# Kernel tuning notes

Hardware: AMD Instinct MI355X
Metric: run time of the kernel (lower is better)

The kernel has to match this reference:

```python
import jax, jax.numpy as jnp
import numpy as np

BETA = 0.35

def setup_inputs() -> dict:
    key = jax.random.key(0)
    k1, k2, k3 = jax.random.split(key, 3)
    B, D, C, O = 16384, 512, 4096, 128
    x = jax.random.normal(k1, (B, D), dtype=jnp.float32)
    centers = jax.random.normal(k2, (C, D), dtype=jnp.float32)
    W = jax.random.normal(k3, (C, O), dtype=jnp.float32) * (1.0 / np.sqrt(C))
    b = jnp.zeros((O,), dtype=jnp.float32)
    return {"x": x, "centers": centers, "W": W, "b": b}

def reference(x, centers, W, b):
    # Squared Euclidean distances via the GEMM identity ||a-b||^2 = ||a||^2 + ||b||^2 - 2 a.b
    # (same math as expand_dims/subtract/square/reduce_sum, avoids [B,C,D] intermediate)
    x_sq = jnp.sum(x * x, axis=1, keepdims=True)          # [B,1]
    c_sq = jnp.sum(centers * centers, axis=1)             # [C]
    cross = x @ centers.T                                  # [B,C]
    sq_dist = x_sq + c_sq[None, :] - 2.0 * cross           # [B,C]
    rbf = jnp.exp(-BETA * sq_dist)                         # [B,C]
    return rbf @ W + b                                      # [B,O]
```

## Files before the change

### kernel.cpp

```cpp
#include <hip/hip_runtime.h>
#include <hip/hip_bf16.h>

typedef short bf16x8 __attribute__((ext_vector_type(8)));
typedef float f32x4 __attribute__((ext_vector_type(4)));
typedef float f32x16 __attribute__((ext_vector_type(16)));
typedef long l64x2 __attribute__((ext_vector_type(2)));
typedef unsigned short u16;
typedef unsigned char u8;

#define NB2 (-0.35f * 1.44269504088896340736f)
#define P2C (0.70f * 1.44269504088896340736f)
#define MF8(a,b,c)  __builtin_amdgcn_mfma_f32_32x32x16_fp8_fp8(a, b, c, 0, 0, 0)
#define MFB(a,b,c)  __builtin_amdgcn_mfma_f32_32x32x16_bf16(a, b, c, 0, 0, 0)

__device__ __forceinline__ u16 f2bf(float f) {
  union { float f; unsigned int u; } v; v.f = f;
  unsigned int x = v.u;
  return (u16)((x + 0x7FFFu + ((x >> 16) & 1u)) >> 16);
}

__device__ __forceinline__ unsigned cvtpk(float lo, float hi) {
  unsigned r;
  asm("v_cvt_pk_bf16_f32 %0, %1, %2" : "=v"(r) : "v"(lo), "v"(hi));
  return r;
}

__device__ __forceinline__ void pswap(unsigned &a, unsigned &b) {
  asm volatile("v_permlane32_swap_b32 %0, %1" : "+v"(a), "+v"(b));
}

__device__ __forceinline__ u8 f2e4m3(float f) {
  unsigned int u = __float_as_uint(f);
  u8 s = (u8)((u >> 24) & 0x80u);
  float a = fabsf(f);
  if (a >= 448.f) return s | 0x7E;
  if (a < 0.015625f) return s | (u8)(int)rintf(a * 512.f);
  unsigned int m = u & 0x7fffffffu;
  unsigned int r = m + 0x7FFFFu + ((m >> 20) & 1u);
  return s | (u8)((((r >> 23) - 120u) << 3) | ((r >> 20) & 7u));
}

__device__ __forceinline__ unsigned int pk4(float a, float b, float c, float d) {
#if __has_builtin(__builtin_amdgcn_cvt_pk_fp8_f32)
  int v = __builtin_amdgcn_cvt_pk_fp8_f32(a, b, 0, false);
  v = __builtin_amdgcn_cvt_pk_fp8_f32(c, d, v, true);
  return (unsigned int)v;
#else
  return (unsigned int)f2e4m3(a) | ((unsigned int)f2e4m3(b) << 8)
       | ((unsigned int)f2e4m3(c) << 16) | ((unsigned int)f2e4m3(d) << 24);
#endif
}

#define GLOAD_LDS(g, l) __builtin_amdgcn_global_load_lds( \
    (const __attribute__((address_space(1))) unsigned int*)(g), \
    (__attribute__((address_space(3))) unsigned int*)(l), 16, 0, 0)

__global__ __launch_bounds__(512)
void prep_x8(const float* __restrict__ src, u8* __restrict__ dst,
             float* __restrict__ sq) {
  const int row = blockIdx.x * 8 + (threadIdx.x >> 6);
  const int i6 = threadIdx.x & 63;
  const float4* p = (const float4*)(src + (size_t)row * 512) + i6 * 2;
  float4 a = p[0], b = p[1];
  float ss = a.x*a.x + a.y*a.y + a.z*a.z + a.w*a.w
           + b.x*b.x + b.y*b.y + b.z*b.z + b.w*b.w;
  uint2 o;
  o.x = pk4(a.x, a.y, a.z, a.w);
  o.y = pk4(b.x, b.y, b.z, b.w);
  const int pp = i6 >> 2, sub = (i6 >> 1) & 1, h = i6 & 1;
  const int l = (h << 5) | (row & 31);
  *(uint2*)(dst + (size_t)(row >> 5) * 16384 + pp * 1024 + l * 16 + sub * 8) = o;
  ss += __shfl_xor(ss, 1);  ss += __shfl_xor(ss, 2);
  ss += __shfl_xor(ss, 4);  ss += __shfl_xor(ss, 8);
  ss += __shfl_xor(ss, 16); ss += __shfl_xor(ss, 32);
  if (i6 == 0) sq[row] = ss;
}

__global__ __launch_bounds__(256)
void prep_cen(const float* __restrict__ cen, u8* __restrict__ cfr,
              float* __restrict__ csq) {
  const int t = threadIdx.x;
  const int c = blockIdx.x * 4 + (t >> 6);
  const int i6 = t & 63;
  const float* p = cen + (size_t)c * 512 + i6 * 8;
  float4 a = *(const float4*)p, b = *(const float4*)(p + 4);
  float ss = a.x*a.x + a.y*a.y + a.z*a.z + a.w*a.w
           + b.x*b.x + b.y*b.y + b.z*b.z + b.w*b.w;
  uint2 o;
  o.x = pk4(a.x, a.y, a.z, a.w);
  o.y = pk4(b.x, b.y, b.z, b.w);
  const int pp = i6 >> 2, sub = (i6 >> 1) & 1, h = i6 & 1;
  const int lc = c & 31;
  const int v = (((lc & 7) * 2 + h) ^ ((lc >> 2) & 1));
  *(uint2*)(cfr + (size_t)(c >> 5) * 16384 + pp * 1024 + (lc >> 3) * 256
            + v * 16 + sub * 8) = o;
  ss += __shfl_xor(ss, 1);  ss += __shfl_xor(ss, 2);
  ss += __shfl_xor(ss, 4);  ss += __shfl_xor(ss, 8);
  ss += __shfl_xor(ss, 16); ss += __shfl_xor(ss, 32);
  if (i6 == 0) csq[c] = ss;
}

__global__ __launch_bounds__(256)
void prep_w(const float* __restrict__ W, u8* __restrict__ wt) {
  __shared__ u16 t_[128 * 66];
  const int c0 = blockIdx.x * 64;
  const int t = threadIdx.x;
#pragma unroll
  for (int it = 0; it < 32; ++it) {
    int idx = it * 256 + t;
    int cl = idx >> 7;
    int o  = idx & 127;
    t_[o * 66 + cl] = f2bf(W[(size_t)(c0 + cl) * 128 + o]);
  }
  __syncthreads();
#pragma unroll
  for (int it = 0; it < 4; ++it) {
    int idx = it * 256 + t;
    int o  = idx >> 3;
    int uu = idx & 7;
    int ch = uu >> 2;
    int kt = (uu >> 1) & 1;
    int h2 = uu & 1;
    int u  = (kt * 2 + h2) ^ ((o >> 1) & 3);
    u16* d = (u16*)(wt + ((size_t)(c0 >> 5) + ch) * 8192 + o * 64 + u * 16);
    const u16* s_ = &t_[o * 66 + ch * 32 + kt * 16 + h2 * 8];
#pragma unroll
    for (int j = 0; j < 8; ++j) d[j] = s_[j];
  }
}

__global__ __launch_bounds__(256)
void init_out(const float* __restrict__ bias, float* __restrict__ out) {
  const int i4 = blockIdx.x * 256 + threadIdx.x;
  float4 b = ((const float4*)bias)[i4 & 31];
  ((float4*)out)[i4] = b;
}

__global__ __launch_bounds__(256, 2)
void rbf_main(const u8* __restrict__ xfs, const u8* __restrict__ cfr,
              const u8* __restrict__ wtgb, const float* __restrict__ csq_g,
              const float* __restrict__ xsq_g, float* __restrict__ out)
{
  __shared__ __align__(16) u8 cs[2][16384];
  __shared__ __align__(16) u8 wt[2][8192];
  __shared__ __align__(16) float csq_l[1024];
  __shared__ __align__(16) float xsq_l[128];

  const int tid = threadIdx.x;
  const int lane = tid & 63;
  const int wv = tid >> 6;
  const int l31 = lane & 31;
  const int h = lane >> 5;
  const int bid = blockIdx.x;
  const int chq = bid & 3;
  const size_t r0 = (size_t)(bid >> 2) * 128;

#define S_CS(cc) do { \
    const u8* sG_ = cfr + ((size_t)(chq * 32 + (cc)) << 14) + tid * 16; \
    u8* sL_ = &cs[(cc) & 1][0] + tid * 16; \
    GLOAD_LDS(sG_,         sL_); \
    GLOAD_LDS(sG_ + 4096,  sL_ + 4096); \
    GLOAD_LDS(sG_ + 8192,  sL_ + 8192); \
    GLOAD_LDS(sG_ + 12288, sL_ + 12288); \
  } while (0)

#define S_W(cc) do { \
    const u8* wg_ = wtgb + ((size_t)(chq * 32 + (cc)) << 13) + tid * 16; \
    u8* wl_ = &wt[(cc) & 1][0] + tid * 16; \
    GLOAD_LDS(wg_,        wl_); \
    GLOAD_LDS(wg_ + 4096, wl_ + 4096); \
  } while (0)

  if (tid < 32) GLOAD_LDS(xsq_g + r0 + tid * 4, xsq_l + tid * 4);
  GLOAD_LDS(csq_g + chq * 1024 + tid * 4, csq_l + tid * 4);
  S_CS(0);
  S_W(0);

  l64x2 xf[16];
  {
    const u8* xb = xfs + ((size_t)((bid >> 2) * 4 + wv)) * 16384 + lane * 16;
#pragma unroll
    for (int p = 0; p < 16; ++p)
      xf[p] = *(const l64x2*)(xb + p * 1024);
  }

  asm volatile("s_waitcnt vmcnt(0)" ::: "memory");
  __builtin_amdgcn_s_barrier();
  __builtin_amdgcn_sched_barrier(0);

  const float xn = NB2 * xsq_l[wv * 32 + l31];

  const int cbase = ((l31 >> 3) & 3) * 256
                  + ((((l31 & 7) * 2 + h) ^ ((l31 >> 2) & 1)) << 4);
  const int wsw = (l31 >> 1) & 3;
  const int wb_o = l31 * 64;
  const int wu0 = ((0 + h) ^ wsw) << 4;
  const int wu1 = ((2 + h) ^ wsw) << 4;

  const f32x16 z16 = {0,0,0,0,0,0,0,0,0,0,0,0,0,0,0,0};
  f32x16 oa0 = z16, oa1 = z16, oa2 = z16, oa3 = z16;

#pragma unroll 1
  for (int cc = 0; cc < 32; ++cc) {
    if (cc < 31) { S_CS(cc + 1); S_W(cc + 1); }
    const u8* csb = &cs[cc & 1][0];

    f32x16 s0 = z16, s1 = z16;
#pragma unroll
    for (int p = 0; p < 16; ++p) {
      l64x2 A = *(const l64x2*)(csb + p * 1024 + cbase);
      __builtin_amdgcn_s_setprio(1);
      if (p & 1) {
        s1 = MF8(A[0], xf[p][0], s1);
        s1 = MF8(A[1], xf[p][1], s1);
      } else {
        s0 = MF8(A[0], xf[p][0], s0);
        s0 = MF8(A[1], xf[p][1], s0);
      }
      __builtin_amdgcn_s_setprio(0);
    }

    f32x4 cq0 = *(const f32x4*)(csq_l + cc * 32 + 0  + 4 * h);
    f32x4 cq1 = *(const f32x4*)(csq_l + cc * 32 + 8  + 4 * h);
    f32x4 cq2 = *(const f32x4*)(csq_l + cc * 32 + 16 + 4 * h);
    f32x4 cq3 = *(const f32x4*)(csq_l + cc * 32 + 24 + 4 * h);
    float e[16];
#pragma unroll
    for (int r = 0; r < 16; ++r) {
      const float cq = (r < 4 ? cq0[r] : r < 8 ? cq1[r - 4] : r < 12 ? cq2[r - 8] : cq3[r - 12]);
      e[r] = __builtin_amdgcn_exp2f(fmaf(s0[r] + s1[r], P2C, fmaf(cq, NB2, xn)));
    }
    unsigned P0 = cvtpk(e[0],  e[1]),  P1 = cvtpk(e[2],  e[3]);
    unsigned P2 = cvtpk(e[4],  e[5]),  P3 = cvtpk(e[6],  e[7]);
    unsigned P4 = cvtpk(e[8],  e[9]),  P5 = cvtpk(e[10], e[11]);
    unsigned P6 = cvtpk(e[12], e[13]), P7 = cvtpk(e[14], e[15]);
    pswap(P0, P2); pswap(P1, P3);
    pswap(P4, P6); pswap(P5, P7);
    union { unsigned u[4]; bf16x8 v; } FA, GA;
    FA.u[0] = P0; FA.u[1] = P1; FA.u[2] = P2; FA.u[3] = P3;
    GA.u[0] = P4; GA.u[1] = P5; GA.u[2] = P6; GA.u[3] = P7;

    {
      const u8* wtb = &wt[cc & 1][0];
      bf16x8 wA0 = *(const bf16x8*)(wtb + wb_o + wu0);
      bf16x8 wB0 = *(const bf16x8*)(wtb + wb_o + wu1);
      bf16x8 wA1 = *(const bf16x8*)(wtb + 2048 + wb_o + wu0);
      bf16x8 wB1 = *(const bf16x8*)(wtb + 2048 + wb_o + wu1);
      __builtin_amdgcn_s_setprio(1);
      oa0 = MFB(FA.v, wA0, oa0);
      oa0 = MFB(GA.v, wB0, oa0);
      oa1 = MFB(FA.v, wA1, oa1);
      oa1 = MFB(GA.v, wB1, oa1);
      __builtin_amdgcn_s_setprio(0);
      bf16x8 wA2 = *(const bf16x8*)(wtb + 4096 + wb_o + wu0);
      bf16x8 wB2 = *(const bf16x8*)(wtb + 4096 + wb_o + wu1);
      bf16x8 wA3 = *(const bf16x8*)(wtb + 6144 + wb_o + wu0);
      bf16x8 wB3 = *(const bf16x8*)(wtb + 6144 + wb_o + wu1);
      __builtin_amdgcn_s_setprio(1);
      oa2 = MFB(FA.v, wA2, oa2);
      oa2 = MFB(GA.v, wB2, oa2);
      oa3 = MFB(FA.v, wA3, oa3);
      oa3 = MFB(GA.v, wB3, oa3);
      __builtin_amdgcn_s_setprio(0);
    }

    asm volatile("s_waitcnt vmcnt(0)" ::: "memory");
    __builtin_amdgcn_s_barrier();
    __builtin_amdgcn_sched_barrier(0);
  }

#pragma unroll
  for (int r = 0; r < 16; ++r) {
    const int m = wv * 32 + (r & 3) + 8 * (r >> 2) + 4 * h;
    float* op = &out[(r0 + m) * 128 + l31];
    atomicAdd(op,      oa0[r]);
    atomicAdd(op + 32, oa1[r]);
    atomicAdd(op + 64, oa2[r]);
    atomicAdd(op + 96, oa3[r]);
  }
#undef S_CS
#undef S_W
}

extern "C" void kernel_launch(void* const* d_in, const int* in_sizes, int n_in,
                              void* d_out, int out_size, void* d_ws, size_t ws_size,
                              hipStream_t stream) {
  (void)in_sizes; (void)n_in; (void)out_size; (void)ws_size;
  const float* x   = (const float*)d_in[0];
  const float* cen = (const float*)d_in[1];
  const float* W   = (const float*)d_in[2];
  const float* b   = (const float*)d_in[3];
  u8* xfs = (u8*)d_ws;
  u8* cfr = xfs + (size_t)16384 * 512;
  u8* wtgb = cfr + (size_t)4096 * 512;
  float* csq = (float*)(wtgb + (size_t)128 * 4096 * 2);
  float* xsq = csq + 4096;
  prep_x8<<<2048, 512, 0, stream>>>(x, xfs, xsq);
  prep_cen<<<1024, 256, 0, stream>>>(cen, cfr, csq);
  prep_w<<<64, 256, 0, stream>>>(W, wtgb);
  init_out<<<2048, 256, 0, stream>>>(b, (float*)d_out);
  rbf_main<<<512, 256, 0, stream>>>(xfs, cfr, wtgb, csq, xsq, (float*)d_out);
}
```

Before: 105.9 us.

## Load W fragments directly into registers and triple-buffer center tiles in LDS

```diff
diff --git a/kernel.cpp b/kernel.cpp
--- a/kernel.cpp
+++ b/kernel.cpp
@@ -120,10 +120,10 @@
     int uu = idx & 7;
     int ch = uu >> 2;
     int kt = (uu >> 1) & 1;
-    int h2 = uu & 1;
-    int u  = (kt * 2 + h2) ^ ((o >> 1) & 3);
-    u16* d = (u16*)(wt + ((size_t)(c0 >> 5) + ch) * 8192 + o * 64 + u * 16);
-    const u16* s_ = &t_[o * 66 + ch * 32 + kt * 16 + h2 * 8];
+    int h  = uu & 1;
+    u16* d = (u16*)(wt + ((size_t)(c0 >> 5) + ch) * 8192 + (o >> 5) * 2048
+                    + kt * 1024 + (h * 32 + (o & 31)) * 16);
+    const u16* s_ = &t_[o * 66 + ch * 32 + kt * 16 + h * 8];
 #pragma unroll
     for (int j = 0; j < 8; ++j) d[j] = s_[j];
   }
@@ -141,8 +141,7 @@
               const u8* __restrict__ wtgb, const float* __restrict__ csq_g,
               const float* __restrict__ xsq_g, float* __restrict__ out)
 {
-  __shared__ __align__(16) u8 cs[2][16384];
-  __shared__ __align__(16) u8 wt[2][8192];
+  __shared__ __align__(16) u8 cs[3][16384];
   __shared__ __align__(16) float csq_l[1024];
   __shared__ __align__(16) float xsq_l[128];
 
@@ -157,24 +156,17 @@
 
 #define S_CS(cc) do { \
     const u8* sG_ = cfr + ((size_t)(chq * 32 + (cc)) << 14) + tid * 16; \
-    u8* sL_ = &cs[(cc) & 1][0] + tid * 16; \
+    u8* sL_ = &cs[(cc) % 3][0] + tid * 16; \
     GLOAD_LDS(sG_,         sL_); \
     GLOAD_LDS(sG_ + 4096,  sL_ + 4096); \
     GLOAD_LDS(sG_ + 8192,  sL_ + 8192); \
     GLOAD_LDS(sG_ + 12288, sL_ + 12288); \
   } while (0)
 
-#define S_W(cc) do { \
-    const u8* wg_ = wtgb + ((size_t)(chq * 32 + (cc)) << 13) + tid * 16; \
-    u8* wl_ = &wt[(cc) & 1][0] + tid * 16; \
-    GLOAD_LDS(wg_,        wl_); \
-    GLOAD_LDS(wg_ + 4096, wl_ + 4096); \
-  } while (0)
-
   if (tid < 32) GLOAD_LDS(xsq_g + r0 + tid * 4, xsq_l + tid * 4);
   GLOAD_LDS(csq_g + chq * 1024 + tid * 4, csq_l + tid * 4);
   S_CS(0);
-  S_W(0);
+  S_CS(1);
 
   l64x2 xf[16];
   {
@@ -192,18 +184,26 @@
 
   const int cbase = ((l31 >> 3) & 3) * 256
                   + ((((l31 & 7) * 2 + h) ^ ((l31 >> 2) & 1)) << 4);
-  const int wsw = (l31 >> 1) & 3;
-  const int wb_o = l31 * 64;
-  const int wu0 = ((0 + h) ^ wsw) << 4;
-  const int wu1 = ((2 + h) ^ wsw) << 4;
 
   const f32x16 z16 = {0,0,0,0,0,0,0,0,0,0,0,0,0,0,0,0};
   f32x16 oa0 = z16, oa1 = z16, oa2 = z16, oa3 = z16;
 
 #pragma unroll 1
   for (int cc = 0; cc < 32; ++cc) {
-    if (cc < 31) { S_CS(cc + 1); S_W(cc + 1); }
-    const u8* csb = &cs[cc & 1][0];
+    const u8* wgb = wtgb + ((size_t)(chq * 32 + cc) << 13) + lane * 16;
+    bf16x8 w00 = *(const bf16x8*)(wgb);
+    bf16x8 w01 = *(const bf16x8*)(wgb + 1024);
+    bf16x8 w10 = *(const bf16x8*)(wgb + 2048);
+    bf16x8 w11 = *(const bf16x8*)(wgb + 3072);
+    bf16x8 w20 = *(const bf16x8*)(wgb + 4096);
+    bf16x8 w21 = *(const bf16x8*)(wgb + 5120);
+    bf16x8 w30 = *(const bf16x8*)(wgb + 6144);
+    bf16x8 w31 = *(const bf16x8*)(wgb + 7168);
+    __builtin_amdgcn_sched_barrier(0);
+    if (cc < 30) S_CS(cc + 2);
+    __builtin_amdgcn_sched_barrier(0);
+
+    const u8* csb = &cs[cc % 3][0];
 
     f32x16 s0 = z16, s1 = z16;
 #pragma unroll
@@ -240,31 +240,20 @@
     FA.u[0] = P0; FA.u[1] = P1; FA.u[2] = P2; FA.u[3] = P3;
     GA.u[0] = P4; GA.u[1] = P5; GA.u[2] = P6; GA.u[3] = P7;
 
-    {
-      const u8* wtb = &wt[cc & 1][0];
-      bf16x8 wA0 = *(const bf16x8*)(wtb + wb_o + wu0);
-      bf16x8 wB0 = *(const bf16x8*)(wtb + wb_o + wu1);
-      bf16x8 wA1 = *(const bf16x8*)(wtb + 2048 + wb_o + wu0);
-      bf16x8 wB1 = *(const bf16x8*)(wtb + 2048 + wb_o + wu1);
-      __builtin_amdgcn_s_setprio(1);
-      oa0 = MFB(FA.v, wA0, oa0);
-      oa0 = MFB(GA.v, wB0, oa0);
-      oa1 = MFB(FA.v, wA1, oa1);
-      oa1 = MFB(GA.v, wB1, oa1);
-      __builtin_amdgcn_s_setprio(0);
-      bf16x8 wA2 = *(const bf16x8*)(wtb + 4096 + wb_o + wu0);
-      bf16x8 wB2 = *(const bf16x8*)(wtb + 4096 + wb_o + wu1);
-      bf16x8 wA3 = *(const bf16x8*)(wtb + 6144 + wb_o + wu0);
-      bf16x8 wB3 = *(const bf16x8*)(wtb + 6144 + wb_o + wu1);
-      __builtin_amdgcn_s_setprio(1);
-      oa2 = MFB(FA.v, wA2, oa2);
-      oa2 = MFB(GA.v, wB2, oa2);
-      oa3 = MFB(FA.v, wA3, oa3);
-      oa3 = MFB(GA.v, wB3, oa3);
-      __builtin_amdgcn_s_setprio(0);
-    }
-
-    asm volatile("s_waitcnt vmcnt(0)" ::: "memory");
+    if (cc < 30) { asm volatile("s_waitcnt vmcnt(4)" ::: "memory"); }
+    else         { asm volatile("s_waitcnt vmcnt(0)" ::: "memory"); }
+    __builtin_amdgcn_sched_barrier(0);
+    __builtin_amdgcn_s_setprio(1);
+    oa0 = MFB(FA.v, w00, oa0);
+    oa0 = MFB(GA.v, w01, oa0);
+    oa1 = MFB(FA.v, w10, oa1);
+    oa1 = MFB(GA.v, w11, oa1);
+    oa2 = MFB(FA.v, w20, oa2);
+    oa2 = MFB(GA.v, w21, oa2);
+    oa3 = MFB(FA.v, w30, oa3);
+    oa3 = MFB(GA.v, w31, oa3);
+    __builtin_amdgcn_s_setprio(0);
+
     __builtin_amdgcn_s_barrier();
     __builtin_amdgcn_sched_barrier(0);
   }
@@ -279,7 +268,6 @@
     atomicAdd(op + 96, oa3[r]);
   }
 #undef S_CS
-#undef S_W
 }
 
 extern "C" void kernel_launch(void* const* d_in, const int* in_sizes, int n_in,
```

After: 109.5 us. +3.4%, slower.

## Use scaled 32x32x64 f8f6f4 MFMA for distance GEMM with repacked fp8 layouts

Applied to the files above, without the earlier changes.

```diff
diff --git a/kernel.cpp b/kernel.cpp
--- a/kernel.cpp
+++ b/kernel.cpp
@@ -5,13 +5,15 @@
 typedef float f32x4 __attribute__((ext_vector_type(4)));
 typedef float f32x16 __attribute__((ext_vector_type(16)));
 typedef long l64x2 __attribute__((ext_vector_type(2)));
+typedef int i32x8 __attribute__((ext_vector_type(8)));
 typedef unsigned short u16;
 typedef unsigned char u8;
 
 #define NB2 (-0.35f * 1.44269504088896340736f)
 #define P2C (0.70f * 1.44269504088896340736f)
-#define MF8(a,b,c)  __builtin_amdgcn_mfma_f32_32x32x16_fp8_fp8(a, b, c, 0, 0, 0)
-#define MFB(a,b,c)  __builtin_amdgcn_mfma_f32_32x32x16_bf16(a, b, c, 0, 0, 0)
+#define MFS(a,b,c) __builtin_amdgcn_mfma_scale_f32_32x32x64_f8f6f4( \
+    a, b, c, 0, 0, 0, 0x7F7F7F7F, 0, 0x7F7F7F7F)
+#define MFB(a,b,c) __builtin_amdgcn_mfma_f32_32x32x16_bf16(a, b, c, 0, 0, 0)
 
 __device__ __forceinline__ u16 f2bf(float f) {
   union { float f; unsigned int u; } v; v.f = f;
@@ -67,9 +69,10 @@
   uint2 o;
   o.x = pk4(a.x, a.y, a.z, a.w);
   o.y = pk4(b.x, b.y, b.z, b.w);
-  const int pp = i6 >> 2, sub = (i6 >> 1) & 1, h = i6 & 1;
-  const int l = (h << 5) | (row & 31);
-  *(uint2*)(dst + (size_t)(row >> 5) * 16384 + pp * 1024 + l * 16 + sub * 8) = o;
+  const int P = i6 >> 3, rem = i6 & 7;
+  const int kh = rem >> 2;
+  const int l = (kh << 5) | (row & 31);
+  *(uint2*)(dst + (size_t)(row >> 5) * 16384 + P * 2048 + l * 32 + (rem & 3) * 8) = o;
   ss += __shfl_xor(ss, 1);  ss += __shfl_xor(ss, 2);
   ss += __shfl_xor(ss, 4);  ss += __shfl_xor(ss, 8);
   ss += __shfl_xor(ss, 16); ss += __shfl_xor(ss, 32);
@@ -89,11 +92,14 @@
   uint2 o;
   o.x = pk4(a.x, a.y, a.z, a.w);
   o.y = pk4(b.x, b.y, b.z, b.w);
-  const int pp = i6 >> 2, sub = (i6 >> 1) & 1, h = i6 & 1;
+  const int P = i6 >> 3, rem = i6 & 7;
+  const int kh = rem >> 2;
   const int lc = c & 31;
-  const int v = (((lc & 7) * 2 + h) ^ ((lc >> 2) & 1));
-  *(uint2*)(cfr + (size_t)(c >> 5) * 16384 + pp * 1024 + (lc >> 3) * 256
-            + v * 16 + sub * 8) = o;
+  const int l = (kh << 5) | lc;
+  const int u = (rem >> 1) & 1;
+  const int sub = rem & 1;
+  const int us = u ^ ((lc >> 2) & 1);
+  *(uint2*)(cfr + (size_t)(c >> 5) * 16384 + P * 2048 + l * 32 + us * 16 + sub * 8) = o;
   ss += __shfl_xor(ss, 1);  ss += __shfl_xor(ss, 2);
   ss += __shfl_xor(ss, 4);  ss += __shfl_xor(ss, 8);
   ss += __shfl_xor(ss, 16); ss += __shfl_xor(ss, 32);
@@ -176,12 +182,16 @@
   S_CS(0);
   S_W(0);
 
-  l64x2 xf[16];
+  i32x8 xf8[8];
   {
-    const u8* xb = xfs + ((size_t)((bid >> 2) * 4 + wv)) * 16384 + lane * 16;
-#pragma unroll
-    for (int p = 0; p < 16; ++p)
-      xf[p] = *(const l64x2*)(xb + p * 1024);
+    const u8* xb = xfs + ((size_t)((bid >> 2) * 4 + wv)) * 16384 + lane * 32;
+#pragma unroll
+    for (int P = 0; P < 8; ++P) {
+      union { l64x2 q[2]; i32x8 v; } t;
+      t.q[0] = *(const l64x2*)(xb + P * 2048);
+      t.q[1] = *(const l64x2*)(xb + P * 2048 + 16);
+      xf8[P] = t.v;
+    }
   }
 
   asm volatile("s_waitcnt vmcnt(0)" ::: "memory");
@@ -190,8 +200,9 @@
 
   const float xn = NB2 * xsq_l[wv * 32 + l31];
 
-  const int cbase = ((l31 >> 3) & 3) * 256
-                  + ((((l31 & 7) * 2 + h) ^ ((l31 >> 2) & 1)) << 4);
+  const int swz = (lane >> 2) & 1;
+  const int alo = lane * 32 + swz * 16;
+  const int ahi = lane * 32 + (swz ^ 1) * 16;
   const int wsw = (l31 >> 1) & 3;
   const int wb_o = l31 * 64;
   const int wu0 = ((0 + h) ^ wsw) << 4;
@@ -207,16 +218,13 @@
 
     f32x16 s0 = z16, s1 = z16;
 #pragma unroll
-    for (int p = 0; p < 16; ++p) {
-      l64x2 A = *(const l64x2*)(csb + p * 1024 + cbase);
+    for (int P = 0; P < 8; ++P) {
+      union { l64x2 q[2]; i32x8 v; } A;
+      A.q[0] = *(const l64x2*)(csb + P * 2048 + alo);
+      A.q[1] = *(const l64x2*)(csb + P * 2048 + ahi);
       __builtin_amdgcn_s_setprio(1);
-      if (p & 1) {
-        s1 = MF8(A[0], xf[p][0], s1);
-        s1 = MF8(A[1], xf[p][1], s1);
-      } else {
-        s0 = MF8(A[0], xf[p][0], s0);
-        s0 = MF8(A[1], xf[p][1], s0);
-      }
+      if (P & 1) s1 = MFS(A.v, xf8[P], s1);
+      else       s0 = MFS(A.v, xf8[P], s0);
       __builtin_amdgcn_s_setprio(0);
     }
 
```

New measurement: 93.51 us. 11.7% less time.
